# Performance work log

Measured on AMD Instinct MI355X. Metric: run time of the kernel, lower is better.

Reference implementation:

```python
import jax, jax.numpy as jnp
import numpy as np

D_IN = 512
EMBED = 256
N = 8192

def setup_inputs() -> dict:
    key = jax.random.key(0)
    ks = jax.random.split(key, 6)
    s_in = 1.0 / np.sqrt(D_IN)
    s_e = 1.0 / np.sqrt(EMBED)
    return {
        "X": jax.random.normal(ks[0], (N, D_IN), dtype=jnp.float32),
        "W_Q": jax.random.uniform(ks[1], (EMBED, D_IN), jnp.float32, -s_in, s_in),
        "W_K": jax.random.uniform(ks[2], (EMBED, D_IN), jnp.float32, -s_in, s_in),
        "W_V": jax.random.uniform(ks[3], (EMBED, D_IN), jnp.float32, -s_in, s_in),
        "head_w": jax.random.uniform(ks[4], (1, EMBED), jnp.float32, -s_e, s_e),
        "head_b": jax.random.uniform(ks[5], (1,), jnp.float32, -s_e, s_e),
    }

def reference(X, W_Q, W_K, W_V, head_w, head_b):
    # Projections: nn.Linear(x) = x @ W.T
    Q = X @ W_Q.T                      # [N, D]
    K = X @ W_K.T                      # [N, D]
    V = X @ W_V.T                      # [N, D]
    A = Q @ K.T                        # [N, N] unnormalized linear attention
    Z = A @ V                          # [N, D]
    preds = Z @ head_w.T + head_b      # [N, 1]
    return preds[:, 0]                 # [N]
```

## Files before the change

kernel.cpp:

```cpp
#include <hip/hip_runtime.h>

#define D_IN 512
#define EMBED 256
#define NBLK 256
#define SCALE 16777216.0f
#define INV_SCALE 5.9604644775390625e-08f

typedef unsigned long long ull;

#define WS_WVP_B 0
#define WS_TFX_B 8192
#define WS_CNT_B 40960
#define WS_RP_B  45056
#define N_ZERO   4097

__global__ __launch_bounds__(64) void k_wv(const float* __restrict__ W_V,
                                           const float* __restrict__ head_w,
                                           float* __restrict__ wvp,
                                           ull* __restrict__ zbase) {
    const int cg  = blockIdx.x & 7;
    const int eg  = blockIdx.x >> 3;
    const int col = cg * 64 + threadIdx.x;
    float acc = 0.f;
    const int e0 = eg * 64;
#pragma unroll 8
    for (int e = e0; e < e0 + 64; ++e) acc += head_w[e] * W_V[(size_t)e * D_IN + col];
    wvp[(size_t)eg * D_IN + col] = acc;

    const int g = blockIdx.x * 64 + threadIdx.x;
    for (int i = g; i < N_ZERO; i += 32 * 64) zbase[i] = 0ull;
}

__global__ __launch_bounds__(512) void k_pass1ur(const float* __restrict__ X,
                                                 const float* __restrict__ wvp,
                                                 const float* __restrict__ W_K,
                                                 const float* __restrict__ W_Q,
                                                 ull* __restrict__ t_fixed,
                                                 ull* __restrict__ counter,
                                                 float* __restrict__ rp) {
    const int tid  = threadIdx.x;
    const int lane = tid & 63;
    const int wid  = tid >> 6;
    const int c0   = lane * 4;
    const int c1   = 256 + lane * 4;

    __shared__ float lds[8][D_IN];
    __shared__ float t_lds[D_IN];
    __shared__ float u_lds[8];
    __shared__ unsigned arrival_s;

    float4 wv0 = {0.f,0.f,0.f,0.f}, wv1 = {0.f,0.f,0.f,0.f};
#pragma unroll
    for (int eg = 0; eg < 4; ++eg) {
        const float4 a = *(const float4*)(wvp + (size_t)eg * D_IN + c0);
        const float4 b = *(const float4*)(wvp + (size_t)eg * D_IN + c1);
        wv0.x += a.x; wv0.y += a.y; wv0.z += a.z; wv0.w += a.w;
        wv1.x += b.x; wv1.y += b.y; wv1.z += b.z; wv1.w += b.w;
    }

    float4 t0 = {0.f,0.f,0.f,0.f};
    float4 t1 = {0.f,0.f,0.f,0.f};
    const int row0 = blockIdx.x * 32 + wid * 4;
#pragma unroll
    for (int r = 0; r < 4; ++r) {
        const float* xr = X + (size_t)(row0 + r) * D_IN;
        const float4 a = *(const float4*)(xr + c0);
        const float4 b = *(const float4*)(xr + c1);
        float p = a.x*wv0.x + a.y*wv0.y + a.z*wv0.z + a.w*wv0.w
                + b.x*wv1.x + b.y*wv1.y + b.z*wv1.z + b.w*wv1.w;
#pragma unroll
        for (int off = 32; off >= 1; off >>= 1) p += __shfl_xor(p, off, 64);
        t0.x += p*a.x; t0.y += p*a.y; t0.z += p*a.z; t0.w += p*a.w;
        t1.x += p*b.x; t1.y += p*b.y; t1.z += p*b.z; t1.w += p*b.w;
    }
    *(float4*)(&lds[wid][c0]) = t0;
    *(float4*)(&lds[wid][c1]) = t1;
    __syncthreads();

    {
        float s = 0.f;
#pragma unroll
        for (int w = 0; w < 8; ++w) s += lds[w][tid];
        const long long v = llrintf(s * SCALE);
        ull old = atomicAdd(&t_fixed[(size_t)(blockIdx.x & 7) * D_IN + tid], (ull)v);
        unsigned keep = (unsigned)old ^ (unsigned)(old >> 32);
        asm volatile("" :: "v"(keep));
    }
    __syncthreads();

    if (tid == 0) arrival_s = (unsigned)atomicAdd(counter, 1ull);
    __syncthreads();
    const unsigned arrival = arrival_s;
    if (arrival < 224u) return;
    const int k = (int)arrival - 224;

    if (tid == 0) {
        while (atomicAdd(counter, 0ull) < 256ull) __builtin_amdgcn_s_sleep(8);
    }
    __syncthreads();

    {
        long long acc = 0;
#pragma unroll
        for (int j = 0; j < 8; ++j)
            acc += (long long)atomicAdd(&t_fixed[(size_t)j * D_IN + tid], 0ull);
        t_lds[tid] = (float)acc * INV_SCALE;
    }
    __syncthreads();

    {
        const int e = 8 * k + wid;
        const float4 ta = *(const float4*)(t_lds + c0);
        const float4 tb = *(const float4*)(t_lds + c1);
        const float4 ka = *(const float4*)(W_K + (size_t)e * D_IN + c0);
        const float4 kb = *(const float4*)(W_K + (size_t)e * D_IN + c1);
        float p = ta.x*ka.x + ta.y*ka.y + ta.z*ka.z + ta.w*ka.w
                + tb.x*kb.x + tb.y*kb.y + tb.z*kb.z + tb.w*kb.w;
#pragma unroll
        for (int off = 32; off >= 1; off >>= 1) p += __shfl_xor(p, off, 64);
        if (lane == 0) u_lds[wid] = p;
    }
    __syncthreads();

    {
        float racc = 0.f;
#pragma unroll
        for (int m = 0; m < 8; ++m)
            racc += u_lds[m] * W_Q[(size_t)(8 * k + m) * D_IN + tid];
        rp[(size_t)k * D_IN + tid] = racc;
    }
}

__global__ __launch_bounds__(512) void k_pass2(const float* __restrict__ X,
                                               const float* __restrict__ rp,
                                               const float* __restrict__ head_b,
                                               float* __restrict__ out) {
    __shared__ float r_lds[D_IN];
    const int tid = threadIdx.x;

    float acc = 0.f;
#pragma unroll 8
    for (int j = 0; j < 32; ++j) acc += rp[(size_t)j * D_IN + tid];
    r_lds[tid] = acc;
    __syncthreads();

    const int lane = tid & 63;
    const int wid  = tid >> 6;
    const int c0   = lane * 4;
    const int c1   = 256 + lane * 4;

    const float4 r0 = *(const float4*)(r_lds + c0);
    const float4 r1 = *(const float4*)(r_lds + c1);
    const float bb  = head_b[0];

    const int row0 = blockIdx.x * 32 + wid * 4;
#pragma unroll
    for (int rr = 0; rr < 4; ++rr) {
        const int row = row0 + rr;
        const float* xr = X + (size_t)row * D_IN;
        const float4 a = *(const float4*)(xr + c0);
        const float4 b = *(const float4*)(xr + c1);
        float p = a.x*r0.x + a.y*r0.y + a.z*r0.z + a.w*r0.w
                + b.x*r1.x + b.y*r1.y + b.z*r1.z + b.w*r1.w;
#pragma unroll
        for (int off = 32; off >= 1; off >>= 1) p += __shfl_xor(p, off, 64);
        if (lane == 0) out[row] = p + bb;
    }
}

extern "C" void kernel_launch(void* const* d_in, const int* in_sizes, int n_in,
                              void* d_out, int out_size, void* d_ws, size_t ws_size,
                              hipStream_t stream) {
    const float* X      = (const float*)d_in[0];
    const float* W_Q    = (const float*)d_in[1];
    const float* W_K    = (const float*)d_in[2];
    const float* W_V    = (const float*)d_in[3];
    const float* head_w = (const float*)d_in[4];
    const float* head_b = (const float*)d_in[5];
    float* out = (float*)d_out;

    char* ws = (char*)d_ws;
    float* wvp   = (float*)(ws + WS_WVP_B);
    ull*   t_fix = (ull*)  (ws + WS_TFX_B);
    ull*   cnt   = (ull*)  (ws + WS_CNT_B);
    float* rp    = (float*)(ws + WS_RP_B);

    k_wv     <<<32,   64,  0, stream>>>(W_V, head_w, wvp, t_fix);
    k_pass1ur<<<NBLK, 512, 0, stream>>>(X, wvp, W_K, W_Q, t_fix, cnt, rp);
    k_pass2  <<<NBLK, 512, 0, stream>>>(X, rp, head_b, out);
}
```

Measured before the change: 24.63 us.

## Fuse W_V reduction, pass1 and pass2 into one persistent kernel with flags

```diff
diff --git a/kernel.cpp b/kernel.cpp
--- a/kernel.cpp
+++ b/kernel.cpp
@@ -1,43 +1,59 @@
 #include <hip/hip_runtime.h>
 
+typedef unsigned long long ull;
+
 #define D_IN 512
-#define EMBED 256
 #define NBLK 256
 #define SCALE 16777216.0f
 #define INV_SCALE 5.9604644775390625e-08f
 
-typedef unsigned long long ull;
-
-#define WS_WVP_B 0
-#define WS_TFX_B 8192
-#define WS_CNT_B 40960
-#define WS_RP_B  45056
-#define N_ZERO   4097
-
-__global__ __launch_bounds__(64) void k_wv(const float* __restrict__ W_V,
-                                           const float* __restrict__ head_w,
-                                           float* __restrict__ wvp,
-                                           ull* __restrict__ zbase) {
-    const int cg  = blockIdx.x & 7;
-    const int eg  = blockIdx.x >> 3;
-    const int col = cg * 64 + threadIdx.x;
-    float acc = 0.f;
-    const int e0 = eg * 64;
-#pragma unroll 8
-    for (int e = e0; e < e0 + 64; ++e) acc += head_w[e] * W_V[(size_t)e * D_IN + col];
-    wvp[(size_t)eg * D_IN + col] = acc;
-
-    const int g = blockIdx.x * 64 + threadIdx.x;
-    for (int i = g; i < N_ZERO; i += 32 * 64) zbase[i] = 0ull;
-}
-
-__global__ __launch_bounds__(512) void k_pass1ur(const float* __restrict__ X,
-                                                 const float* __restrict__ wvp,
-                                                 const float* __restrict__ W_K,
-                                                 const float* __restrict__ W_Q,
-                                                 ull* __restrict__ t_fixed,
-                                                 ull* __restrict__ counter,
-                                                 float* __restrict__ rp) {
+#define AG __HIP_MEMORY_SCOPE_AGENT
+
+#define WS_TFX   0
+#define WS_CNT   32768
+#define WS_WVP   33024
+#define WS_WV    98560
+#define WS_RP    100608
+#define WS_R     166144
+#define N_ZERO   4128
+
+__device__ __forceinline__ void fstore_cg(float* p, float v) {
+    __hip_atomic_store((unsigned*)p, __builtin_bit_cast(unsigned, v),
+                       __ATOMIC_RELAXED, AG);
+}
+__device__ __forceinline__ float fload_cg(const float* p) {
+    unsigned u = __hip_atomic_load((const unsigned*)p, __ATOMIC_RELAXED, AG);
+    return __builtin_bit_cast(float, u);
+}
+
+__global__ __launch_bounds__(256) void k_init(ull* __restrict__ z) {
+    int i = blockIdx.x * 256 + threadIdx.x;
+    for (; i < N_ZERO; i += 16 * 256) z[i] = 0ull;
+}
+
+__global__ __launch_bounds__(512) void k_mega(
+    const float* __restrict__ X,
+    const float* __restrict__ W_Q,
+    const float* __restrict__ W_K,
+    const float* __restrict__ W_V,
+    const float* __restrict__ head_w,
+    const float* __restrict__ head_b,
+    float* __restrict__ out,
+    char* __restrict__ ws)
+{
+    ull*   t_fixed = (ull*)(ws + WS_TFX);
+    ull*   cnts    = (ull*)(ws + WS_CNT);
+    ull*   wv_cnt  = cnts + 0;
+    ull*   wv_done = cnts + 1;
+    ull*   t_cnt   = cnts + 2;
+    ull*   rp_cnt  = cnts + 3;
+    ull*   r_done  = cnts + 4;
+    float* wvp     = (float*)(ws + WS_WVP);
+    float* wv      = (float*)(ws + WS_WV);
+    float* rp      = (float*)(ws + WS_RP);
+    float* rv      = (float*)(ws + WS_R);
+
+    const int b    = blockIdx.x;
     const int tid  = threadIdx.x;
     const int lane = tid & 63;
     const int wid  = tid >> 6;
@@ -47,124 +63,157 @@
     __shared__ float lds[8][D_IN];
     __shared__ float t_lds[D_IN];
     __shared__ float u_lds[8];
-    __shared__ unsigned arrival_s;
-
-    float4 wv0 = {0.f,0.f,0.f,0.f}, wv1 = {0.f,0.f,0.f,0.f};
-#pragma unroll
-    for (int eg = 0; eg < 4; ++eg) {
-        const float4 a = *(const float4*)(wvp + (size_t)eg * D_IN + c0);
-        const float4 b = *(const float4*)(wvp + (size_t)eg * D_IN + c1);
-        wv0.x += a.x; wv0.y += a.y; wv0.z += a.z; wv0.w += a.w;
-        wv1.x += b.x; wv1.y += b.y; wv1.z += b.z; wv1.w += b.w;
-    }
+    __shared__ unsigned flag_s;
+
+    float4 xa[4], xb[4];
+    const int row0 = b * 32 + wid * 4;
+#pragma unroll
+    for (int r = 0; r < 4; ++r) {
+        const float* xr = X + (size_t)(row0 + r) * D_IN;
+        xa[r] = *(const float4*)(xr + c0);
+        xb[r] = *(const float4*)(xr + c1);
+    }
+
+    if (b < 32) {
+        float acc = 0.f;
+#pragma unroll
+        for (int m = 0; m < 8; ++m)
+            acc += head_w[b * 8 + m] * W_V[(size_t)(b * 8 + m) * D_IN + tid];
+        fstore_cg(&wvp[(size_t)b * D_IN + tid], acc);
+        __syncthreads();
+        if (tid == 0) {
+            ull old = __hip_atomic_fetch_add(wv_cnt, 1ull, __ATOMIC_ACQ_REL, AG);
+            flag_s = (old == 31ull) ? 1u : 0u;
+        }
+        __syncthreads();
+        if (flag_s) {
+            float s = 0.f;
+#pragma unroll 8
+            for (int j = 0; j < 32; ++j) s += fload_cg(&wvp[(size_t)j * D_IN + tid]);
+            fstore_cg(&wv[tid], s);
+            __syncthreads();
+            if (tid == 0) __hip_atomic_store(wv_done, 1ull, __ATOMIC_RELEASE, AG);
+        }
+    }
+
+    if (tid == 0) {
+        while (__hip_atomic_load(wv_done, __ATOMIC_ACQUIRE, AG) == 0ull)
+            __builtin_amdgcn_s_sleep(2);
+    }
+    __syncthreads();
+
+    float4 wv0, wv1;
+    wv0.x = fload_cg(&wv[c0+0]); wv0.y = fload_cg(&wv[c0+1]);
+    wv0.z = fload_cg(&wv[c0+2]); wv0.w = fload_cg(&wv[c0+3]);
+    wv1.x = fload_cg(&wv[c1+0]); wv1.y = fload_cg(&wv[c1+1]);
+    wv1.z = fload_cg(&wv[c1+2]); wv1.w = fload_cg(&wv[c1+3]);
 
     float4 t0 = {0.f,0.f,0.f,0.f};
     float4 t1 = {0.f,0.f,0.f,0.f};
-    const int row0 = blockIdx.x * 32 + wid * 4;
 #pragma unroll
     for (int r = 0; r < 4; ++r) {
-        const float* xr = X + (size_t)(row0 + r) * D_IN;
-        const float4 a = *(const float4*)(xr + c0);
-        const float4 b = *(const float4*)(xr + c1);
-        float p = a.x*wv0.x + a.y*wv0.y + a.z*wv0.z + a.w*wv0.w
-                + b.x*wv1.x + b.y*wv1.y + b.z*wv1.z + b.w*wv1.w;
+        float p = xa[r].x*wv0.x + xa[r].y*wv0.y + xa[r].z*wv0.z + xa[r].w*wv0.w
+                + xb[r].x*wv1.x + xb[r].y*wv1.y + xb[r].z*wv1.z + xb[r].w*wv1.w;
 #pragma unroll
         for (int off = 32; off >= 1; off >>= 1) p += __shfl_xor(p, off, 64);
-        t0.x += p*a.x; t0.y += p*a.y; t0.z += p*a.z; t0.w += p*a.w;
-        t1.x += p*b.x; t1.y += p*b.y; t1.z += p*b.z; t1.w += p*b.w;
+        t0.x += p*xa[r].x; t0.y += p*xa[r].y; t0.z += p*xa[r].z; t0.w += p*xa[r].w;
+        t1.x += p*xb[r].x; t1.y += p*xb[r].y; t1.z += p*xb[r].z; t1.w += p*xb[r].w;
     }
     *(float4*)(&lds[wid][c0]) = t0;
     *(float4*)(&lds[wid][c1]) = t1;
     __syncthreads();
-
     {
         float s = 0.f;
 #pragma unroll
         for (int w = 0; w < 8; ++w) s += lds[w][tid];
         const long long v = llrintf(s * SCALE);
-        ull old = atomicAdd(&t_fixed[(size_t)(blockIdx.x & 7) * D_IN + tid], (ull)v);
+        ull old = __hip_atomic_fetch_add(&t_fixed[(size_t)(b & 7) * D_IN + tid],
+                                         (ull)v, __ATOMIC_RELAXED, AG);
         unsigned keep = (unsigned)old ^ (unsigned)(old >> 32);
         asm volatile("" :: "v"(keep));
     }
     __syncthreads();
 
-    if (tid == 0) arrival_s = (unsigned)atomicAdd(counter, 1ull);
-    __syncthreads();
-    const unsigned arrival = arrival_s;
-    if (arrival < 224u) return;
-    const int k = (int)arrival - 224;
-
     if (tid == 0) {
-        while (atomicAdd(counter, 0ull) < 256ull) __builtin_amdgcn_s_sleep(8);
-    }
-    __syncthreads();
-
-    {
+        ull old = __hip_atomic_fetch_add(t_cnt, 1ull, __ATOMIC_ACQ_REL, AG);
+        flag_s = (unsigned)old;
+    }
+    __syncthreads();
+    const unsigned arrival = flag_s;
+
+    if (arrival >= 224u) {
+        const int k = (int)arrival - 224;
+        if (tid == 0) {
+            while (__hip_atomic_load(t_cnt, __ATOMIC_ACQUIRE, AG) < 256ull)
+                __builtin_amdgcn_s_sleep(2);
+        }
+        __syncthreads();
+
         long long acc = 0;
 #pragma unroll
         for (int j = 0; j < 8; ++j)
-            acc += (long long)atomicAdd(&t_fixed[(size_t)j * D_IN + tid], 0ull);
+            acc += (long long)__hip_atomic_load(&t_fixed[(size_t)j * D_IN + tid],
+                                                __ATOMIC_RELAXED, AG);
         t_lds[tid] = (float)acc * INV_SCALE;
-    }
-    __syncthreads();
-
-    {
-        const int e = 8 * k + wid;
-        const float4 ta = *(const float4*)(t_lds + c0);
-        const float4 tb = *(const float4*)(t_lds + c1);
-        const float4 ka = *(const float4*)(W_K + (size_t)e * D_IN + c0);
-        const float4 kb = *(const float4*)(W_K + (size_t)e * D_IN + c1);
-        float p = ta.x*ka.x + ta.y*ka.y + ta.z*ka.z + ta.w*ka.w
-                + tb.x*kb.x + tb.y*kb.y + tb.z*kb.z + tb.w*kb.w;
+        __syncthreads();
+
+        {
+            const int e = 8 * k + wid;
+            const float4 ta = *(const float4*)(t_lds + c0);
+            const float4 tb = *(const float4*)(t_lds + c1);
+            const float4 ka = *(const float4*)(W_K + (size_t)e * D_IN + c0);
+            const float4 kb = *(const float4*)(W_K + (size_t)e * D_IN + c1);
+            float p = ta.x*ka.x + ta.y*ka.y + ta.z*ka.z + ta.w*ka.w
+                    + tb.x*kb.x + tb.y*kb.y + tb.z*kb.z + tb.w*kb.w;
+#pragma unroll
+            for (int off = 32; off >= 1; off >>= 1) p += __shfl_xor(p, off, 64);
+            if (lane == 0) u_lds[wid] = p;
+        }
+        __syncthreads();
+
+        {
+            float racc = 0.f;
+#pragma unroll
+            for (int m = 0; m < 8; ++m)
+                racc += u_lds[m] * W_Q[(size_t)(8 * k + m) * D_IN + tid];
+            fstore_cg(&rp[(size_t)k * D_IN + tid], racc);
+        }
+        __syncthreads();
+        if (tid == 0) {
+            ull old = __hip_atomic_fetch_add(rp_cnt, 1ull, __ATOMIC_ACQ_REL, AG);
+            flag_s = (old == 31ull) ? 1u : 0u;
+        }
+        __syncthreads();
+        if (flag_s) {
+            float s = 0.f;
+#pragma unroll 8
+            for (int j = 0; j < 32; ++j) s += fload_cg(&rp[(size_t)j * D_IN + tid]);
+            fstore_cg(&rv[tid], s);
+            __syncthreads();
+            if (tid == 0) __hip_atomic_store(r_done, 1ull, __ATOMIC_RELEASE, AG);
+        }
+    }
+
+    if (tid == 0) {
+        while (__hip_atomic_load(r_done, __ATOMIC_ACQUIRE, AG) == 0ull)
+            __builtin_amdgcn_s_sleep(2);
+    }
+    __syncthreads();
+
+    float4 r0, r1;
+    r0.x = fload_cg(&rv[c0+0]); r0.y = fload_cg(&rv[c0+1]);
+    r0.z = fload_cg(&rv[c0+2]); r0.w = fload_cg(&rv[c0+3]);
+    r1.x = fload_cg(&rv[c1+0]); r1.y = fload_cg(&rv[c1+1]);
+    r1.z = fload_cg(&rv[c1+2]); r1.w = fload_cg(&rv[c1+3]);
+    const float bb = head_b[0];
+
+#pragma unroll
+    for (int r = 0; r < 4; ++r) {
+        float p = xa[r].x*r0.x + xa[r].y*r0.y + xa[r].z*r0.z + xa[r].w*r0.w
+                + xb[r].x*r1.x + xb[r].y*r1.y + xb[r].z*r1.z + xb[r].w*r1.w;
 #pragma unroll
         for (int off = 32; off >= 1; off >>= 1) p += __shfl_xor(p, off, 64);
-        if (lane == 0) u_lds[wid] = p;
-    }
-    __syncthreads();
-
-    {
-        float racc = 0.f;
-#pragma unroll
-        for (int m = 0; m < 8; ++m)
-            racc += u_lds[m] * W_Q[(size_t)(8 * k + m) * D_IN + tid];
-        rp[(size_t)k * D_IN + tid] = racc;
-    }
-}
-
-__global__ __launch_bounds__(512) void k_pass2(const float* __restrict__ X,
-                                               const float* __restrict__ rp,
-                                               const float* __restrict__ head_b,
-                                               float* __restrict__ out) {
-    __shared__ float r_lds[D_IN];
-    const int tid = threadIdx.x;
-
-    float acc = 0.f;
-#pragma unroll 8
-    for (int j = 0; j < 32; ++j) acc += rp[(size_t)j * D_IN + tid];
-    r_lds[tid] = acc;
-    __syncthreads();
-
-    const int lane = tid & 63;
-    const int wid  = tid >> 6;
-    const int c0   = lane * 4;
-    const int c1   = 256 + lane * 4;
-
-    const float4 r0 = *(const float4*)(r_lds + c0);
-    const float4 r1 = *(const float4*)(r_lds + c1);
-    const float bb  = head_b[0];
-
-    const int row0 = blockIdx.x * 32 + wid * 4;
-#pragma unroll
-    for (int rr = 0; rr < 4; ++rr) {
-        const int row = row0 + rr;
-        const float* xr = X + (size_t)row * D_IN;
-        const float4 a = *(const float4*)(xr + c0);
-        const float4 b = *(const float4*)(xr + c1);
-        float p = a.x*r0.x + a.y*r0.y + a.z*r0.z + a.w*r0.w
-                + b.x*r1.x + b.y*r1.y + b.z*r1.z + b.w*r1.w;
-#pragma unroll
-        for (int off = 32; off >= 1; off >>= 1) p += __shfl_xor(p, off, 64);
-        if (lane == 0) out[row] = p + bb;
+        if (lane == 0) out[row0 + r] = p + bb;
     }
 }
 
@@ -178,14 +227,8 @@
     const float* head_w = (const float*)d_in[4];
     const float* head_b = (const float*)d_in[5];
     float* out = (float*)d_out;
-
-    char* ws = (char*)d_ws;
-    float* wvp   = (float*)(ws + WS_WVP_B);
-    ull*   t_fix = (ull*)  (ws + WS_TFX_B);
-    ull*   cnt   = (ull*)  (ws + WS_CNT_B);
-    float* rp    = (float*)(ws + WS_RP_B);
-
-    k_wv     <<<32,   64,  0, stream>>>(W_V, head_w, wvp, t_fix);
-    k_pass1ur<<<NBLK, 512, 0, stream>>>(X, wvp, W_K, W_Q, t_fix, cnt, rp);
-    k_pass2  <<<NBLK, 512, 0, stream>>>(X, rp, head_b, out);
-}
+    char* ws   = (char*)d_ws;
+
+    k_init<<<16,   256, 0, stream>>>((ull*)ws);
+    k_mega<<<NBLK, 512, 0, stream>>>(X, W_Q, W_K, W_V, head_w, head_b, out, ws);
+}
```

Result: slower. 77.52 us (+214.8%).
